# Optimization experiments

Hardware: AMD Instinct MI355X
Metric: run time of the kernel (lower is better)

## Reference

```python
import jax, jax.numpy as jnp
import numpy as np

DIM = 1024
DIM_HEAD = 64
N_HEADS = 16
CTX = 2048
BATCH = 4
EPS = 1e-5


def _alibi_M(ctx, n_heads):
    # head_scalars = 2**(-8/n) for n = [n_heads, ..., 1]
    scalars = 2.0 ** (-8.0 / np.arange(n_heads, 0, -1, dtype=np.float64))
    idx = np.arange(ctx)
    dist = -np.abs(idx[:, None] - idx[None, :]).astype(np.float64)  # [ctx, ctx]
    return jnp.asarray(scalars[:, None, None] * dist[None], dtype=jnp.float32)  # [h, ctx, ctx]


def setup_inputs() -> dict:
    key = jax.random.key(0)
    ks = jax.random.split(key, 6)
    inner = DIM_HEAD * N_HEADS
    s = 1.0 / np.sqrt(DIM)
    return {
        "x": jax.random.normal(ks[0], (BATCH, CTX, DIM), dtype=jnp.float32),
        "ln_w": jnp.ones((DIM,), dtype=jnp.float32),
        "ln_b": jnp.zeros((DIM,), dtype=jnp.float32),
        "Wq": jax.random.normal(ks[1], (DIM, inner), dtype=jnp.float32) * s,
        "Wk": jax.random.normal(ks[2], (DIM, inner), dtype=jnp.float32) * s,
        "Wv": jax.random.normal(ks[3], (DIM, inner), dtype=jnp.float32) * s,
        "Wo": jax.random.normal(ks[4], (inner, DIM), dtype=jnp.float32) * s,
        "M": _alibi_M(CTX, N_HEADS),
    }


def reference(x, ln_w, ln_b, Wq, Wk, Wv, Wo, M):
    # LayerNorm
    mu = jnp.mean(x, axis=-1, keepdims=True)
    var = jnp.mean(jnp.square(x - mu), axis=-1, keepdims=True)
    xn = (x - mu) * jax.lax.rsqrt(var + EPS) * ln_w + ln_b

    b, n, _ = xn.shape

    def heads(t):  # [b, n, h*d] -> [b, h, n, d]
        return t.reshape(b, n, N_HEADS, DIM_HEAD).transpose(0, 2, 1, 3)

    q = heads(xn @ Wq)
    k = heads(xn @ Wk)
    v = heads(xn @ Wv)

    scores = jnp.einsum("bhid,bhjd->bhij", q, k) / jnp.sqrt(jnp.float32(DIM_HEAD))
    scores = scores + M[None, :, :n, :n]  # ALiBi bias
    attn = jax.nn.softmax(scores, axis=-1)

    out = jnp.einsum("bhij,bhjd->bhid", attn, v)
    out = out.transpose(0, 2, 1, 3).reshape(b, n, N_HEADS * DIM_HEAD)
    return out @ Wo
```

## Files before the change

kernel.cpp:

```cpp
#include <hip/hip_runtime.h>

using s16x8  = __attribute__((ext_vector_type(8)))  short;
using s16x4  = __attribute__((ext_vector_type(4)))  short;
using f32x4  = __attribute__((ext_vector_type(4)))  float;
using f32x16 = __attribute__((ext_vector_type(16))) float;
using u32 = unsigned int;

#define LOG2E  1.4426950408889634f
#define QSCALE 0.18033688011112042f

static __device__ __forceinline__ ushort f2bf(float f) {
    union { float f; unsigned u; } c; c.f = f;
    unsigned u = c.u;
    unsigned r = (u + 0x7fffu + ((u >> 16) & 1u)) >> 16;
    return (ushort)r;
}
static __device__ __forceinline__ float bf2f(ushort h) {
    union { unsigned u; float f; } c; c.u = ((unsigned)h) << 16;
    return c.f;
}
static __device__ __forceinline__ u32 cvt_pk_bf16(float a, float b) {
    u32 r;
    asm("v_cvt_pk_bf16_f32 %0, %1, %2" : "=v"(r) : "v"(a), "v"(b));
    return r;
}
static __device__ __forceinline__ void permlane32_swap(u32& a, u32& b) {
    asm volatile("v_permlane32_swap_b32 %0, %1" : "+v"(a), "+v"(b));
}
static __device__ __forceinline__ f32x16 mfma32(s16x8 a, s16x8 b, f32x16 c) {
    return __builtin_amdgcn_mfma_f32_32x32x16_bf16(a, b, c, 0, 0, 0);
}
typedef __attribute__((address_space(3))) void lds_vt;
typedef __attribute__((address_space(1))) const void glb_vt;
static __device__ __forceinline__ void gload16(const void* g, void* l) {
    __builtin_amdgcn_global_load_lds((glb_vt*)g, (lds_vt*)l, 16, 0, 0);
}

#define PACKFRAG(p, base, out) {                              \
    u32 a0 = cvt_pk_bf16(p[base+0], p[base+1]);               \
    u32 b0 = cvt_pk_bf16(p[base+4], p[base+5]);               \
    permlane32_swap(a0, b0);                                  \
    u32 a1 = cvt_pk_bf16(p[base+2], p[base+3]);               \
    u32 b1 = cvt_pk_bf16(p[base+6], p[base+7]);               \
    permlane32_swap(a1, b1);                                  \
    union { u32 u[4]; s16x8 v; } f_;                          \
    f_.u[0] = a0; f_.u[1] = a1; f_.u[2] = b0; f_.u[3] = b1;   \
    out = f_.v; }

__global__ __launch_bounds__(256) void wprep4_kernel(const float* __restrict__ W0,
                                                     const float* __restrict__ W1,
                                                     const float* __restrict__ W2,
                                                     const float* __restrict__ W3,
                                                     ushort* __restrict__ wqkv,
                                                     ushort* __restrict__ wot) {
    __shared__ float tile[32][33];
    const int z = blockIdx.z;
    const float* W = (z == 0) ? W0 : (z == 1) ? W1 : (z == 2) ? W2 : W3;
    ushort* Wt = (z < 3) ? (wqkv + ((size_t)z << 20)) : wot;
    const float scale = (z == 0) ? QSCALE : 1.0f;
    const int k0 = blockIdx.x * 32, n0 = blockIdx.y * 32;
    const int tx = threadIdx.x & 31, ty = threadIdx.x >> 5;
    #pragma unroll
    for (int i = 0; i < 32; i += 8)
        tile[ty + i][tx] = W[(size_t)(k0 + ty + i) * 1024 + n0 + tx];
    __syncthreads();
    #pragma unroll
    for (int i = 0; i < 32; i += 8)
        Wt[(size_t)(n0 + ty + i) * 1024 + k0 + tx] = f2bf(tile[tx][ty + i] * scale);
}

__global__ __launch_bounds__(256) void ln_kernel(const float* __restrict__ x,
                                                 const float* __restrict__ w,
                                                 const float* __restrict__ b,
                                                 ushort* __restrict__ xn) {
    const int row = blockIdx.x;
    const float4 v = ((const float4*)(x + (size_t)row * 1024))[threadIdx.x];
    float s  = v.x + v.y + v.z + v.w;
    float s2 = v.x * v.x + v.y * v.y + v.z * v.z + v.w * v.w;
    #pragma unroll
    for (int off = 1; off < 64; off <<= 1) {
        s  += __shfl_xor(s, off);
        s2 += __shfl_xor(s2, off);
    }
    __shared__ float red[8];
    const int wid = threadIdx.x >> 6, lane = threadIdx.x & 63;
    if (lane == 0) { red[wid] = s; red[4 + wid] = s2; }
    __syncthreads();
    s  = red[0] + red[1] + red[2] + red[3];
    s2 = red[4] + red[5] + red[6] + red[7];
    const float mu = s * (1.0f / 1024.0f);
    const float var = s2 * (1.0f / 1024.0f) - mu * mu;
    const float rstd = rsqrtf(var + 1e-5f);
    const float4 wv = ((const float4*)w)[threadIdx.x];
    const float4 bv = ((const float4*)b)[threadIdx.x];
    s16x4 o;
    o[0] = (short)f2bf((v.x - mu) * rstd * wv.x + bv.x);
    o[1] = (short)f2bf((v.y - mu) * rstd * wv.y + bv.y);
    o[2] = (short)f2bf((v.z - mu) * rstd * wv.z + bv.z);
    o[3] = (short)f2bf((v.w - mu) * rstd * wv.w + bv.w);
    ((s16x4*)xn)[(size_t)row * 256 + threadIdx.x] = o;
}

__global__ __launch_bounds__(256) void gemm_kernel(const ushort* __restrict__ A,
                                                   const ushort* __restrict__ Wt,
                                                   ushort* __restrict__ oq,
                                                   float* __restrict__ of,
                                                   int nblkn, int omode) {
    __shared__ ushort As[128 * 32];
    __shared__ ushort Bs[128 * 32];

    const int nwg = gridDim.x;
    const int cpx = nwg >> 3;
    const int bid = blockIdx.x;
    const int logical = (bid & 7) * cpx + (bid >> 3);
    const int mb = logical / nblkn, nb = logical % nblkn;
    const int m0 = mb * 128, n0 = nb * 128;

    const int wid = threadIdx.x >> 6, lane = threadIdx.x & 63;
    const int l15 = lane & 15, lg = lane >> 4;
    const int wm = (wid >> 1) * 64, wn = (wid & 1) * 64;

    const int trow = threadIdx.x >> 2;
    const int tchk = threadIdx.x & 3;
    const ushort* ga0 = A  + (size_t)(m0 + trow) * 1024 + tchk * 8;
    const ushort* ga1 = ga0 + 64 * 1024;
    const ushort* gb0 = Wt + (size_t)(n0 + trow) * 1024 + tchk * 8;
    const ushort* gb1 = gb0 + 64 * 1024;
    ushort* lA = As + wid * 512;
    ushort* lB = Bs + wid * 512;

    f32x4 acc[4][4] = {};
    for (int k0 = 0; k0 < 1024; k0 += 32) {
        __syncthreads();
        gload16(ga0 + k0, lA);
        gload16(ga1 + k0, lA + 2048);
        gload16(gb0 + k0, lB);
        gload16(gb1 + k0, lB + 2048);
        __syncthreads();
        s16x8 af[4], bf[4];
        #pragma unroll
        for (int mi = 0; mi < 4; ++mi)
            af[mi] = *(const s16x8*)(As + (wm + mi * 16 + l15) * 32 + lg * 8);
        #pragma unroll
        for (int ni = 0; ni < 4; ++ni)
            bf[ni] = *(const s16x8*)(Bs + (wn + ni * 16 + l15) * 32 + lg * 8);
        #pragma unroll
        for (int mi = 0; mi < 4; ++mi)
            #pragma unroll
            for (int ni = 0; ni < 4; ++ni)
                acc[mi][ni] = __builtin_amdgcn_mfma_f32_16x16x32_bf16(af[mi], bf[ni], acc[mi][ni], 0, 0, 0);
    }

    #pragma unroll
    for (int mi = 0; mi < 4; ++mi) {
        #pragma unroll
        for (int ni = 0; ni < 4; ++ni) {
            const int row = m0 + wm + mi * 16 + lg * 4;
            const int col = n0 + wn + ni * 16 + l15;
            if (omode == 0) {
                const int tcol = col >> 10;
                const int h = (col >> 6) & 15, d = col & 63;
                const int bb = row >> 11, i = row & 2047;
                const int bhv = bb * 16 + h;
                if (tcol == 0) {
                    ushort* o = oq + ((((size_t)bhv) * 2048 + i) * 64 + d);
                    #pragma unroll
                    for (int r = 0; r < 4; ++r) o[(size_t)r * 64] = f2bf(acc[mi][ni][r]);
                } else if (tcol == 1) {
                    const int tt = i >> 6, half = (i >> 5) & 1, l31 = i & 31;
                    const int c = d >> 4, hi2 = (d >> 3) & 1, e = d & 7;
                    ushort* o = oq + ((size_t)1 << 23)
                              + ((size_t)(bhv * 32 + tt)) * 8192
                              + half * 2048 + c * 512 + (hi2 * 32 + l31) * 8 + e;
                    #pragma unroll
                    for (int r = 0; r < 4; ++r) o[r * 8] = f2bf(acc[mi][ni][r]);
                } else {
                    const int tt = i >> 6, jc = (i >> 3) & 7, e0 = i & 7;
                    const int s2 = ((jc >> 2) << 1) | ((jc >> 1) & 1), hi2 = jc & 1;
                    const int half = d >> 5, l31 = d & 31;
                    ushort* o = oq + ((size_t)1 << 23)
                              + ((size_t)(bhv * 32 + tt)) * 8192 + 4096
                              + half * 2048 + s2 * 512 + (hi2 * 32 + l31) * 8 + e0;
                    s16x4 pk;
                    #pragma unroll
                    for (int r = 0; r < 4; ++r) pk[r] = (short)f2bf(acc[mi][ni][r]);
                    *(s16x4*)o = pk;
                }
            } else {
                #pragma unroll
                for (int r = 0; r < 4; ++r) of[(size_t)(row + r) * 1024 + col] = acc[mi][ni][r];
            }
        }
    }
}

__global__ __launch_bounds__(256, 4) void attn_kernel(const ushort* __restrict__ Q,
                                                      const ushort* __restrict__ KV,
                                                      ushort* __restrict__ O) {
    __shared__ __align__(16) char lds[32768];

    const int bid = blockIdx.x;
    const int logical = (bid & 7) * 128 + (bid >> 3);
    const int bh = logical >> 4;
    const int b = bh >> 4, h = bh & 15;
    const int q0 = (logical & 15) * 128;

    const int wid = threadIdx.x >> 6, lane = threadIdx.x & 63;
    const int l31 = lane & 31, hi = lane >> 5;
    const float slope2 = exp2f(-8.0f / (float)(16 - h)) * LOG2E;

    const ushort* Qh  = Q + (size_t)bh * (2048 * 64);
    const ushort* kvsp = KV + (size_t)bh * 262144 + (size_t)(wid * 64 + lane) * 8;
    char* sdst = lds + wid * 1024;

    const int qw = q0 + wid * 32;
    const int qi = qw + l31;
    const float qif = (float)qi;
    const float fq4 = (float)(qi - 4 * hi);

    s16x8 qf[4];
    #pragma unroll
    for (int c = 0; c < 4; ++c)
        qf[c] = *(const s16x8*)(Qh + (size_t)qi * 64 + c * 16 + hi * 8);

    const u32 hmask = hi ? 0u : 0xFFFFFFFFu;
    union { u32 u[4]; s16x8 v; } kxa, kxb;
    kxa.u[0] = cvt_pk_bf16((float)l31 - 32.f, (float)l31 - 32.f) & hmask;
    kxa.u[1] = 0x3F803F80u & hmask; kxa.u[2] = 0; kxa.u[3] = 0;
    kxb.u[0] = cvt_pk_bf16((float)l31, (float)l31) & hmask;
    kxb.u[1] = kxa.u[1]; kxb.u[2] = 0; kxb.u[3] = 0;
    const float s2h = bf2f(f2bf(slope2));
    const float s2l = slope2 - s2h;
    const u32 wpos = ((u32)f2bf(s2l) << 16) | (u32)f2bf(s2h);
    const u32 wneg = wpos ^ 0x80008000u;

    f32x16 oacc0 = {}, oacc1 = {};
    float lsum = 0.0f;

#define STAGE(tt, bb) { \
        const ushort* s_ = kvsp + (size_t)(tt) * 8192; \
        char* d_ = sdst + (bb) * 16384; \
        gload16(s_,        d_); \
        gload16(s_ + 2048, d_ + 4096); \
        gload16(s_ + 4096, d_ + 8192); \
        gload16(s_ + 6144, d_ + 12288); \
    }

    STAGE(0, 0);

    for (int t = 0; t < 32; ++t) {
        const int cur = t & 1;
        const int j0 = t * 64;

        if (t < 31) {
            STAGE(t + 1, cur ^ 1);
            asm volatile("s_waitcnt vmcnt(4)" ::: "memory");
        } else {
            asm volatile("s_waitcnt vmcnt(0)" ::: "memory");
        }
        asm volatile("s_barrier" ::: "memory");

        const char* Kl = lds + cur * 16384;

        s16x8 kf[8];
        #pragma unroll
        for (int c = 0; c < 4; ++c) {
            kf[c]     = *(const s16x8*)(Kl + c * 1024 + lane * 16);
            kf[4 + c] = *(const s16x8*)(Kl + 4096 + c * 1024 + lane * 16);
        }

        f32x16 sa0 = {}, sa1 = {};
        __builtin_amdgcn_s_setprio(1);
        #pragma unroll
        for (int c = 0; c < 4; ++c) {
            sa0 = mfma32(kf[c], qf[c], sa0);
            sa1 = mfma32(kf[4 + c], qf[c], sa1);
        }
        __builtin_amdgcn_s_setprio(0);

        const bool strad = (j0 > qw - 64) && (j0 < qw + 32);
        float ps = 0.0f;
        if (!strad) {
            const bool left = (j0 < qw);
            const float v = (left ? -slope2 : slope2) * (qif - (float)(j0 + 32));
            const u32 pk0 = cvt_pk_bf16(v, 0.f);
            union { u32 u; float f; } vh; vh.u = pk0 << 16;
            union { u32 u[4]; s16x8 v8; } qx;
            qx.u[0] = (left ? wpos : wneg) & hmask;
            qx.u[1] = cvt_pk_bf16(vh.f, v - vh.f) & hmask;
            qx.u[2] = 0; qx.u[3] = 0;
            sa0 = mfma32(kxa.v, qx.v8, sa0);
            sa1 = mfma32(kxb.v, qx.v8, sa1);
            #pragma unroll
            for (int r = 0; r < 16; ++r) {
                sa0[r] = __builtin_amdgcn_exp2f(sa0[r]);
                sa1[r] = __builtin_amdgcn_exp2f(sa1[r]);
                ps += sa0[r] + sa1[r];
            }
        } else {
            const float base0 = fq4 - (float)j0;
            #pragma unroll
            for (int r = 0; r < 16; ++r) {
                const float C = (float)((r & 3) + 8 * (r >> 2));
                sa0[r] = __builtin_amdgcn_exp2f(fmaf(-slope2, fabsf(base0 - C), sa0[r]));
                sa1[r] = __builtin_amdgcn_exp2f(fmaf(-slope2, fabsf(base0 - 32.f - C), sa1[r]));
                ps += sa0[r] + sa1[r];
            }
        }
        lsum += ps;

        s16x8 pb00, pb01, pb10, pb11;
        PACKFRAG(sa0, 0, pb00);  PACKFRAG(sa0, 8, pb01);
        PACKFRAG(sa1, 0, pb10);  PACKFRAG(sa1, 8, pb11);

        s16x8 vf[8];
        #pragma unroll
        for (int s2i = 0; s2i < 4; ++s2i) {
            vf[s2i]     = *(const s16x8*)(Kl + 8192 + s2i * 1024 + lane * 16);
            vf[4 + s2i] = *(const s16x8*)(Kl + 12288 + s2i * 1024 + lane * 16);
        }
        __builtin_amdgcn_s_setprio(1);
        #pragma unroll
        for (int s = 0; s < 2; ++s) {
            #pragma unroll
            for (int kc = 0; kc < 2; ++kc) {
                const s16x8 pw = (s == 0) ? (kc == 0 ? pb00 : pb01)
                                          : (kc == 0 ? pb10 : pb11);
                oacc0 = mfma32(vf[s * 2 + kc], pw, oacc0);
                oacc1 = mfma32(vf[4 + s * 2 + kc], pw, oacc1);
            }
        }
        __builtin_amdgcn_s_setprio(0);

        asm volatile("s_barrier" ::: "memory");
    }
#undef STAGE

    const float lt = lsum + __shfl_xor(lsum, 32);
    const float inv = 1.0f / lt;

    char* ep = lds + wid * 4096;
    #pragma unroll
    for (int dt = 0; dt < 2; ++dt) {
        #pragma unroll
        for (int pr = 0; pr < 8; ++pr) {
            const float va = (dt ? oacc1[2 * pr] : oacc0[2 * pr]) * inv;
            const float vb = (dt ? oacc1[2 * pr + 1] : oacc0[2 * pr + 1]) * inv;
            const u32 w = cvt_pk_bf16(va, vb);
            const int d0 = dt * 32 + ((2 * pr) & 3) + 8 * (pr >> 1) + 4 * hi;
            const int byte = l31 * 128 + ((d0 * 2) ^ ((l31 & 7) << 4));
            *(u32*)(ep + byte) = w;
        }
    }
    __syncthreads();
    #pragma unroll
    for (int rr = 0; rr < 4; ++rr) {
        const int row = (lane >> 3) + rr * 8;
        const int c16 = (lane & 7) ^ (row & 7);
        const s16x8 v = *(const s16x8*)(ep + row * 128 + c16 * 16);
        *(s16x8*)(O + ((size_t)(b * 2048 + qw + row)) * 1024 + h * 64 + (lane & 7) * 8) = v;
    }
}

extern "C" void kernel_launch(void* const* d_in, const int* in_sizes, int n_in,
                              void* d_out, int out_size, void* d_ws, size_t ws_size,
                              hipStream_t stream) {
    (void)in_sizes; (void)n_in; (void)out_size; (void)ws_size;
    const float* x   = (const float*)d_in[0];
    const float* lnw = (const float*)d_in[1];
    const float* lnb = (const float*)d_in[2];
    const float* Wq  = (const float*)d_in[3];
    const float* Wk  = (const float*)d_in[4];
    const float* Wv  = (const float*)d_in[5];
    const float* Wo  = (const float*)d_in[6];

    char* w = (char*)d_ws;
    ushort* xn   = (ushort*)(w);
    ushort* wqkv = (ushort*)(w + (16u << 20));
    ushort* wot  = (ushort*)(w + (22u << 20));
    ushort* Qb   = (ushort*)(w + (24u << 20));

    wprep4_kernel<<<dim3(32, 32, 4), 256, 0, stream>>>(Wq, Wk, Wv, Wo, wqkv, wot);
    ln_kernel<<<dim3(8192), 256, 0, stream>>>(x, lnw, lnb, xn);

    gemm_kernel<<<dim3(1536), 256, 0, stream>>>(xn, wqkv, Qb, nullptr, 24, 0);

    attn_kernel<<<dim3(1024), 256, 0, stream>>>(Qb, Qb + ((size_t)1 << 23), xn);

    gemm_kernel<<<dim3(512), 256, 0, stream>>>(xn, wot, nullptr, (float*)d_out, 8, 1);
}
```

Baseline: 219.4 us.

## Double-buffer LDS tiles in projection GEMM to overlap global loads with MFMA

The projection GEMM now uses two LDS stages. It prefetches the next K-slice with direct-to-LDS loads while the current slice is consumed, synchronising with explicit vmcnt waits and barriers instead of two __syncthreads per iteration. It also raises wave priority around the MFMA block. The aim is to hide global-load latency in the QKV and output projections, at the cost of doubling the GEMM's LDS to 32KB, which may reduce occupancy.

```diff
diff --git a/kernel.cpp b/kernel.cpp
--- a/kernel.cpp
+++ b/kernel.cpp
@@ -106,8 +106,7 @@
                                                    ushort* __restrict__ oq,
                                                    float* __restrict__ of,
                                                    int nblkn, int omode) {
-    __shared__ ushort As[128 * 32];
-    __shared__ ushort Bs[128 * 32];
+    __shared__ __align__(16) char glds[32768];
 
     const int nwg = gridDim.x;
     const int cpx = nwg >> 3;
@@ -126,30 +125,49 @@
     const ushort* ga1 = ga0 + 64 * 1024;
     const ushort* gb0 = Wt + (size_t)(n0 + trow) * 1024 + tchk * 8;
     const ushort* gb1 = gb0 + 64 * 1024;
-    ushort* lA = As + wid * 512;
-    ushort* lB = Bs + wid * 512;
+    char* lA = glds + wid * 1024;
+    char* lB = glds + 8192 + wid * 1024;
+
+#define GSTAGE(kk, bb) { \
+        const int o_ = (bb) * 16384; \
+        gload16(ga0 + (kk), lA + o_); \
+        gload16(ga1 + (kk), lA + o_ + 4096); \
+        gload16(gb0 + (kk), lB + o_); \
+        gload16(gb1 + (kk), lB + o_ + 4096); \
+    }
 
     f32x4 acc[4][4] = {};
+    GSTAGE(0, 0);
     for (int k0 = 0; k0 < 1024; k0 += 32) {
-        __syncthreads();
-        gload16(ga0 + k0, lA);
-        gload16(ga1 + k0, lA + 2048);
-        gload16(gb0 + k0, lB);
-        gload16(gb1 + k0, lB + 2048);
-        __syncthreads();
+        const int cur = (k0 >> 5) & 1;
+        if (k0 < 992) {
+            GSTAGE(k0 + 32, cur ^ 1);
+            asm volatile("s_waitcnt vmcnt(4)" ::: "memory");
+        } else {
+            asm volatile("s_waitcnt vmcnt(0)" ::: "memory");
+        }
+        asm volatile("s_barrier" ::: "memory");
+
+        const char* As = glds + cur * 16384;
+        const char* Bs = As + 8192;
         s16x8 af[4], bf[4];
         #pragma unroll
         for (int mi = 0; mi < 4; ++mi)
-            af[mi] = *(const s16x8*)(As + (wm + mi * 16 + l15) * 32 + lg * 8);
+            af[mi] = *(const s16x8*)(As + (wm + mi * 16 + l15) * 64 + lg * 16);
         #pragma unroll
         for (int ni = 0; ni < 4; ++ni)
-            bf[ni] = *(const s16x8*)(Bs + (wn + ni * 16 + l15) * 32 + lg * 8);
+            bf[ni] = *(const s16x8*)(Bs + (wn + ni * 16 + l15) * 64 + lg * 16);
+        __builtin_amdgcn_s_setprio(1);
         #pragma unroll
         for (int mi = 0; mi < 4; ++mi)
             #pragma unroll
             for (int ni = 0; ni < 4; ++ni)
                 acc[mi][ni] = __builtin_amdgcn_mfma_f32_16x16x32_bf16(af[mi], bf[ni], acc[mi][ni], 0, 0, 0);
-    }
+        __builtin_amdgcn_s_setprio(0);
+
+        asm volatile("s_barrier" ::: "memory");
+    }
+#undef GSTAGE
 
     #pragma unroll
     for (int mi = 0; mi < 4; ++mi) {
```

Measured after the change: 211.3 us. 3.7% less time.
